# Kernel optimization log

Measured on AMD Instinct MI355X. Metric: run time of the kernel, lower is better.

## Reference

```python
import jax, jax.numpy as jnp
import numpy as np

B, N, D, H, DK, DV = 2, 2048, 1024, 16, 64, 64
NEG = -1000000000.0
EPS = 1e-6


def setup_inputs() -> dict:
    key = jax.random.key(0)
    ks = jax.random.split(key, 8)
    s = 0.02
    return {
        "q": jax.random.normal(ks[0], (B, N, D), jnp.float32),
        "k": jax.random.normal(ks[1], (B, N, D), jnp.float32),
        "v": jax.random.normal(ks[2], (B, N, D), jnp.float32),
        "attn_mask": jnp.ones((B, N, N), jnp.int32),
        "Wq": jax.random.normal(ks[3], (D, H * DK), jnp.float32) * s,
        "Wk": jax.random.normal(ks[4], (D, H * DK), jnp.float32) * s,
        "Wv": jax.random.normal(ks[5], (D, H * DV), jnp.float32) * s,
        "Wo": jax.random.normal(ks[6], (H * DV, D), jnp.float32) * s,
        "gamma": jnp.ones((D,), jnp.float32),
        "beta": jnp.zeros((D,), jnp.float32),
    }


def reference(q, k, v, attn_mask, Wq, Wk, Wv, Wo, gamma, beta):
    b, n, _ = q.shape
    residual = q
    # project and split heads: (b, h, n, dk)
    qh = (q @ Wq).reshape(b, n, H, DK).transpose(0, 2, 1, 3)
    kh = (k @ Wk).reshape(b, n, H, DK).transpose(0, 2, 1, 3)
    vh = (v @ Wv).reshape(b, n, H, DV).transpose(0, 2, 1, 3)
    temperature = DK ** 0.5
    scores = jnp.einsum('bhnd,bhmd->bhnm', qh / temperature, kh)
    # external mask (masked where mask == 0), broadcast over heads
    scores = jnp.where(attn_mask[:, None, :, :] == 0, NEG, scores)
    # built-in causal mask (strictly upper triangle)
    causal = jnp.triu(jnp.ones((n, n), dtype=bool), k=1)
    scores = jnp.where(causal, NEG, scores)
    attn = jax.nn.softmax(scores, axis=-1)
    out = jnp.einsum('bhnm,bhmd->bnhd', attn, vh).reshape(b, n, H * DV)
    out = out @ Wo + residual
    # LayerNorm(eps=1e-6)
    mean = out.mean(-1, keepdims=True)
    var = ((out - mean) ** 2).mean(-1, keepdims=True)
    out = (out - mean) / jnp.sqrt(var + EPS) * gamma + beta
    return out, attn
```

## Files before the change

### kernel.cpp

```cpp
#include <hip/hip_runtime.h>
#include <hip/hip_bf16.h>
#include <stdint.h>

#define B_ 2
#define N_ 2048
#define D_ 1024
#define H_ 16
#define MM 4096
#define NN 1024
#define KK 1024

typedef __bf16 bf16;
typedef __bf16 bf16x8 __attribute__((ext_vector_type(8)));
typedef float f32x4 __attribute__((ext_vector_type(4)));

struct __align__(8) bf4 { bf16 v[4]; };

#define LDS_STRIDE 144

__global__ void k_wtt(const float* __restrict__ W, bf16* __restrict__ Wt) {
    __shared__ float t[32][33];
    int bx = blockIdx.x * 32, by = blockIdx.y * 32;
    int tx = threadIdx.x, ty = threadIdx.y;
#pragma unroll
    for (int j = 0; j < 32; j += 8)
        t[ty + j][tx] = W[(size_t)(by + ty + j) * 1024 + bx + tx];
    __syncthreads();
#pragma unroll
    for (int j = 0; j < 32; j += 8)
        Wt[(size_t)(bx + ty + j) * 1024 + by + tx] = (bf16)t[tx][ty + j];
}

__global__ __launch_bounds__(256) void k_bits(const int* __restrict__ mask,
                                              uint32_t* __restrict__ bits) {
    size_t flat = (size_t)blockIdx.x * 256 + threadIdx.x;
    int col = (int)(flat & (N_ - 1));
    int row = (int)((flat >> 11) & (N_ - 1));
    bool ok = (mask[flat] != 0) && (col <= row);
    unsigned long long bal = __ballot(ok);
    if ((threadIdx.x & 63) == 0)
        *(unsigned long long*)(bits + (flat >> 5)) = bal;
}

template <int MODE, bool AF32>
__global__ __launch_bounds__(256) void k_gemm(const void* __restrict__ Av,
                                              const bf16* __restrict__ Bt,
                                              bf16* __restrict__ Cb,
                                              float* __restrict__ Cf,
                                              const float* __restrict__ resid,
                                              float scale) {
    __shared__ __align__(16) char AsB[64 * LDS_STRIDE];
    __shared__ __align__(16) char BsB[128 * LDS_STRIDE];
    const int tid = threadIdx.x, lane = tid & 63, w = tid >> 6;
    const int g = lane >> 4, li = lane & 15;
    const int bm0 = blockIdx.x * 64, bn0 = blockIdx.y * 128;
    const int srow = tid >> 3, sc = tid & 7;
    const bf16* Ab = (const bf16*)Av;
    const float* Af = (const float*)Av;

    f32x4 zz = {0.f, 0.f, 0.f, 0.f};
    f32x4 acc[4][2];
#pragma unroll
    for (int mf = 0; mf < 4; ++mf)
#pragma unroll
        for (int nf = 0; nf < 2; ++nf) acc[mf][nf] = zz;

    f32x4 pa0[2], pa1[2];
    bf16x8 pab[2];
    bf16x8 pb[4];

    auto issueA = [&](int k0) {
        if constexpr (AF32) {
#pragma unroll
            for (int i = 0; i < 2; ++i) {
                const float* s = Af + (size_t)(bm0 + srow + 32 * i) * KK + k0 + sc * 8;
                pa0[i] = *(const f32x4*)s;
                pa1[i] = *(const f32x4*)(s + 4);
            }
        } else {
#pragma unroll
            for (int i = 0; i < 2; ++i)
                pab[i] = *(const bf16x8*)(Ab + (size_t)(bm0 + srow + 32 * i) * KK + k0 + sc * 8);
        }
    };
    auto issueB = [&](int k0) {
#pragma unroll
        for (int i = 0; i < 4; ++i)
            pb[i] = *(const bf16x8*)(Bt + (size_t)(bn0 + srow + 32 * i) * KK + k0 + sc * 8);
    };
    auto writeS = [&]() {
#pragma unroll
        for (int i = 0; i < 2; ++i) {
            bf16x8 t;
            if constexpr (AF32) {
#pragma unroll
                for (int j = 0; j < 4; ++j) {
                    t[j] = (bf16)pa0[i][j];
                    t[4 + j] = (bf16)pa1[i][j];
                }
            } else {
                t = pab[i];
            }
            *(bf16x8*)(AsB + (srow + 32 * i) * LDS_STRIDE + sc * 16) = t;
        }
#pragma unroll
        for (int i = 0; i < 4; ++i)
            *(bf16x8*)(BsB + (srow + 32 * i) * LDS_STRIDE + sc * 16) = pb[i];
    };

    issueA(0);
    issueB(0);
    for (int k0 = 0; k0 < KK; k0 += 64) {
        __syncthreads();
        writeS();
        int kn = (k0 + 64 < KK) ? k0 + 64 : k0;
        issueA(kn);
        issueB(kn);
        __syncthreads();
#pragma unroll
        for (int kk = 0; kk < 2; ++kk) {
            const int kb = kk * 64 + (g << 4);
            bf16x8 bfr[2];
#pragma unroll
            for (int nf = 0; nf < 2; ++nf) {
                int rn = w * 32 + nf * 16 + li;
                bfr[nf] = *(const bf16x8*)(BsB + rn * LDS_STRIDE + kb);
            }
#pragma unroll
            for (int mf = 0; mf < 4; ++mf) {
                int rm = mf * 16 + li;
                bf16x8 afr = *(const bf16x8*)(AsB + rm * LDS_STRIDE + kb);
                acc[mf][0] = __builtin_amdgcn_mfma_f32_16x16x32_bf16(
                    afr, bfr[0], acc[mf][0], 0, 0, 0);
                acc[mf][1] = __builtin_amdgcn_mfma_f32_16x16x32_bf16(
                    afr, bfr[1], acc[mf][1], 0, 0, 0);
            }
        }
    }
#pragma unroll
    for (int mf = 0; mf < 4; ++mf)
#pragma unroll
        for (int nf = 0; nf < 2; ++nf) {
            int n = bn0 + w * 32 + nf * 16 + li;
            int m0 = bm0 + mf * 16 + (g << 2);
            if (MODE == 0) {
#pragma unroll
                for (int r = 0; r < 4; ++r)
                    Cb[(size_t)(m0 + r) * NN + n] = (bf16)(acc[mf][nf][r] * scale);
            } else if (MODE == 1) {
                int bq = m0 >> 11, tok = m0 & (N_ - 1);
                int hh = n >> 6, dv = n & 63;
                bf4 val;
#pragma unroll
                for (int r = 0; r < 4; ++r) val.v[r] = (bf16)(acc[mf][nf][r] * scale);
                *(bf4*)(Cb + ((size_t)((bq * H_ + hh) * 64 + dv)) * N_ + tok) = val;
            } else {
#pragma unroll
                for (int r = 0; r < 4; ++r) {
                    size_t ix = (size_t)(m0 + r) * NN + n;
                    Cf[ix] = acc[mf][nf][r] + resid[ix];
                }
            }
        }
}

__global__ __launch_bounds__(256) void k_attn(const bf16* __restrict__ Qh,
                                              const bf16* __restrict__ Kh,
                                              const bf16* __restrict__ Vt,
                                              const uint32_t* __restrict__ bits,
                                              float* __restrict__ attnp,
                                              bf16* __restrict__ Ob) {
    __shared__ __align__(16) char Qs[64 * LDS_STRIDE];
    __shared__ __align__(16) char Ks[64 * LDS_STRIDE];
    __shared__ __align__(16) char Vs[64 * LDS_STRIDE];
    __shared__ __align__(16) char Ps[64 * LDS_STRIDE];
    const int tid = threadIdx.x, lane = tid & 63, w = tid >> 6;
    const int g = lane >> 4, li = lane & 15;
    const int p = blockIdx.x, h = blockIdx.y, b = blockIdx.z;
    const int srow = tid >> 3, sc = tid & 7;
    const int myrow = w * 16 + li;

    const size_t kbase = ((size_t)b * N_) * D_ + h * 64;
    const size_t vbase = ((size_t)(b * H_ + h) * 64) * N_;
    f32x4 zz = {0.f, 0.f, 0.f, 0.f};

    for (int half = 0; half < 2; ++half) {
        const int qt = half ? (31 - p) : p;
        const int i0 = qt << 6;
        const size_t abase = (((size_t)b * H_ + h) * N_ + i0) * (size_t)N_;

        __syncthreads();
        {
            const char* qsrc = (const char*)Qh +
                (kbase + (size_t)(i0 + srow) * D_ + sc * 8) * 2;
            bf16x8 t0 = *(const bf16x8*)qsrc;
            bf16x8 t1 = *(const bf16x8*)(qsrc + (size_t)32 * D_ * 2);
            *(bf16x8*)(Qs + srow * LDS_STRIDE + sc * 16) = t0;
            *(bf16x8*)(Qs + (srow + 32) * LDS_STRIDE + sc * 16) = t1;
        }
        const uint32_t* mrow = bits + (((size_t)b * N_ + i0 + myrow) << 6);

        float m = -1e30f, l = 0.f;
        bf16x8 ka, kb2;
        {
            const char* ks = (const char*)Kh + (kbase + (size_t)srow * D_ + sc * 8) * 2;
            ka = *(const bf16x8*)ks;
            kb2 = *(const bf16x8*)(ks + (size_t)32 * D_ * 2);
        }
        for (int jt = 0; jt <= qt; ++jt) {
            __syncthreads();
            *(bf16x8*)(Ks + srow * LDS_STRIDE + sc * 16) = ka;
            *(bf16x8*)(Ks + (srow + 32) * LDS_STRIDE + sc * 16) = kb2;
            {
                int jn = (jt < qt) ? jt + 1 : qt;
                const char* ks = (const char*)Kh +
                    (kbase + (size_t)(jn * 64 + srow) * D_ + sc * 8) * 2;
                ka = *(const bf16x8*)ks;
                kb2 = *(const bf16x8*)(ks + (size_t)32 * D_ * 2);
            }
            uint2 mw = *(const uint2*)(mrow + (jt << 1));
            __syncthreads();

            f32x4 s[4];
#pragma unroll
            for (int mf = 0; mf < 4; ++mf) s[mf] = zz;
#pragma unroll
            for (int kk = 0; kk < 2; ++kk) {
                const int kb = kk * 64 + (g << 4);
                bf16x8 qf = *(const bf16x8*)(Qs + myrow * LDS_STRIDE + kb);
#pragma unroll
                for (int mf = 0; mf < 4; ++mf) {
                    bf16x8 kf = *(const bf16x8*)(Ks + (mf * 16 + li) * LDS_STRIDE + kb);
                    s[mf] = __builtin_amdgcn_mfma_f32_16x16x32_bf16(kf, qf, s[mf], 0, 0, 0);
                }
            }
            float tmax = m;
#pragma unroll
            for (int mf = 0; mf < 4; ++mf) {
                uint32_t wsel = (mf < 2) ? mw.x : mw.y;
#pragma unroll
                for (int r = 0; r < 4; ++r) {
                    int sh = (mf & 1) * 16 + g * 4 + r;
                    float xv = ((wsel >> sh) & 1) ? s[mf][r] : -1e9f;
                    s[mf][r] = xv;
                    tmax = fmaxf(tmax, xv);
                }
            }
            tmax = fmaxf(tmax, __shfl_xor(tmax, 16));
            tmax = fmaxf(tmax, __shfl_xor(tmax, 32));
            float ps = 0.f;
#pragma unroll
            for (int mf = 0; mf < 4; ++mf)
#pragma unroll
                for (int r = 0; r < 4; ++r) ps += __expf(s[mf][r] - tmax);
            ps += __shfl_xor(ps, 16);
            ps += __shfl_xor(ps, 32);
            l = l * __expf(m - tmax) + ps;
            m = tmax;
        }
        const float linv = 1.0f / l;

        f32x4 oacc[4];
#pragma unroll
        for (int nf = 0; nf < 4; ++nf) oacc[nf] = zz;

        bf16x8 va, vb2;
        {
            const char* ks = (const char*)Kh + (kbase + (size_t)srow * D_ + sc * 8) * 2;
            ka = *(const bf16x8*)ks;
            kb2 = *(const bf16x8*)(ks + (size_t)32 * D_ * 2);
            const char* vs = (const char*)Vt + (vbase + (size_t)srow * N_ + sc * 8) * 2;
            va = *(const bf16x8*)vs;
            vb2 = *(const bf16x8*)(vs + (size_t)32 * N_ * 2);
        }
        for (int jt = 0; jt <= qt; ++jt) {
            __syncthreads();
            *(bf16x8*)(Ks + srow * LDS_STRIDE + sc * 16) = ka;
            *(bf16x8*)(Ks + (srow + 32) * LDS_STRIDE + sc * 16) = kb2;
            *(bf16x8*)(Vs + srow * LDS_STRIDE + sc * 16) = va;
            *(bf16x8*)(Vs + (srow + 32) * LDS_STRIDE + sc * 16) = vb2;
            {
                int jn = (jt < qt) ? jt + 1 : qt;
                const char* ks = (const char*)Kh +
                    (kbase + (size_t)(jn * 64 + srow) * D_ + sc * 8) * 2;
                ka = *(const bf16x8*)ks;
                kb2 = *(const bf16x8*)(ks + (size_t)32 * D_ * 2);
                const char* vs = (const char*)Vt +
                    (vbase + (size_t)srow * N_ + jn * 64 + sc * 8) * 2;
                va = *(const bf16x8*)vs;
                vb2 = *(const bf16x8*)(vs + (size_t)32 * N_ * 2);
            }
            uint2 mw = *(const uint2*)(mrow + (jt << 1));
            __syncthreads();

            f32x4 s[4];
#pragma unroll
            for (int mf = 0; mf < 4; ++mf) s[mf] = zz;
#pragma unroll
            for (int kk = 0; kk < 2; ++kk) {
                const int kb = kk * 64 + (g << 4);
                bf16x8 qf = *(const bf16x8*)(Qs + myrow * LDS_STRIDE + kb);
#pragma unroll
                for (int mf = 0; mf < 4; ++mf) {
                    bf16x8 kf = *(const bf16x8*)(Ks + (mf * 16 + li) * LDS_STRIDE + kb);
                    s[mf] = __builtin_amdgcn_mfma_f32_16x16x32_bf16(kf, qf, s[mf], 0, 0, 0);
                }
            }
#pragma unroll
            for (int mf = 0; mf < 4; ++mf) {
                uint32_t wsel = (mf < 2) ? mw.x : mw.y;
#pragma unroll
                for (int r = 0; r < 4; ++r) {
                    int sh = (mf & 1) * 16 + g * 4 + r;
                    float xv = ((wsel >> sh) & 1) ? s[mf][r] : -1e9f;
                    s[mf][r] = __expf(xv - m) * linv;
                }
                *(f32x4*)(attnp + abase + (size_t)myrow * N_ + (jt << 6) + mf * 16 + g * 4) = s[mf];
                bf4 pk;
#pragma unroll
                for (int r = 0; r < 4; ++r) pk.v[r] = (bf16)s[mf][r];
                *(bf4*)(Ps + myrow * LDS_STRIDE + (mf * 16 + g * 4) * 2) = pk;
            }
#pragma unroll
            for (int kk = 0; kk < 2; ++kk) {
                const int kb = kk * 64 + (g << 4);
                bf16x8 pf = *(const bf16x8*)(Ps + myrow * LDS_STRIDE + kb);
#pragma unroll
                for (int nf = 0; nf < 4; ++nf) {
                    bf16x8 vf = *(const bf16x8*)(Vs + (nf * 16 + li) * LDS_STRIDE + kb);
                    oacc[nf] = __builtin_amdgcn_mfma_f32_16x16x32_bf16(pf, vf, oacc[nf], 0, 0, 0);
                }
            }
        }
#pragma unroll
        for (int nf = 0; nf < 4; ++nf)
#pragma unroll
            for (int r = 0; r < 4; ++r) {
                int gi = i0 + w * 16 + g * 4 + r;
                Ob[((size_t)(b * N_ + gi)) * D_ + h * 64 + nf * 16 + li] = (bf16)oacc[nf][r];
            }
        int zc0 = i0 + 64;
        if (zc0 < N_) {
            int r = tid >> 2, tc = tid & 3;
            f32x4 z = zz;
            for (int c = zc0 + tc * 4; c < N_; c += 16)
                *(f32x4*)(attnp + abase + (size_t)r * N_ + c) = z;
        }
    }
}

__global__ __launch_bounds__(256) void k_ln(float* __restrict__ out,
                                            const float* __restrict__ gamma,
                                            const float* __restrict__ beta) {
    const int row = blockIdx.x, t = threadIdx.x, lane = t & 63, w = t >> 6;
    float* p = out + (size_t)row * D_;
    f32x4 x = *(const f32x4*)(p + t * 4);
    float s = x[0] + x[1] + x[2] + x[3];
    float s2 = x[0] * x[0] + x[1] * x[1] + x[2] * x[2] + x[3] * x[3];
#pragma unroll
    for (int o = 1; o < 64; o <<= 1) {
        s += __shfl_xor(s, o);
        s2 += __shfl_xor(s2, o);
    }
    __shared__ float r1[4], r2[4];
    if (lane == 0) { r1[w] = s; r2[w] = s2; }
    __syncthreads();
    s = r1[0] + r1[1] + r1[2] + r1[3];
    s2 = r2[0] + r2[1] + r2[2] + r2[3];
    float mean = s * (1.f / D_);
    float var = s2 * (1.f / D_) - mean * mean;
    float rstd = rsqrtf(var + 1e-6f);
    f32x4 gv = *(const f32x4*)(gamma + t * 4);
    f32x4 bv = *(const f32x4*)(beta + t * 4);
    f32x4 y;
#pragma unroll
    for (int c = 0; c < 4; ++c) y[c] = (x[c] - mean) * rstd * gv[c] + bv[c];
    *(f32x4*)(p + t * 4) = y;
}

extern "C" void kernel_launch(void* const* d_in, const int* in_sizes, int n_in,
                              void* d_out, int out_size, void* d_ws,
                              size_t ws_size, hipStream_t stream) {
    (void)in_sizes; (void)n_in; (void)out_size; (void)ws_size;
    const float* q = (const float*)d_in[0];
    const float* k = (const float*)d_in[1];
    const float* v = (const float*)d_in[2];
    const int* msk = (const int*)d_in[3];
    const float* Wq = (const float*)d_in[4];
    const float* Wk = (const float*)d_in[5];
    const float* Wv = (const float*)d_in[6];
    const float* Wo = (const float*)d_in[7];
    const float* gamma = (const float*)d_in[8];
    const float* beta = (const float*)d_in[9];

    float* outp = (float*)d_out;
    float* attnp = outp + (size_t)B_ * N_ * D_;

    const size_t U = (size_t)B_ * N_ * D_;
    const size_t W1 = (size_t)D_ * D_;
    bf16* ws = (bf16*)d_ws;
    bf16* WqT = ws;  ws += W1;
    bf16* WkT = ws;  ws += W1;
    bf16* WvT = ws;  ws += W1;
    bf16* WoT = ws;  ws += W1;
    bf16* Qh = ws;   ws += U;
    bf16* Kh = ws;   ws += U;
    bf16* Vt = ws;   ws += U;
    bf16* Ob = ws;   ws += U;
    uint32_t* bits = (uint32_t*)ws;

    dim3 tb(32, 8);
    k_wtt<<<dim3(32, 32), tb, 0, stream>>>(Wq, WqT);
    k_wtt<<<dim3(32, 32), tb, 0, stream>>>(Wk, WkT);
    k_wtt<<<dim3(32, 32), tb, 0, stream>>>(Wv, WvT);
    k_wtt<<<dim3(32, 32), tb, 0, stream>>>(Wo, WoT);
    k_bits<<<(size_t)B_ * N_ * N_ / 256, 256, 0, stream>>>(msk, bits);

    dim3 gg(MM / 64, NN / 128);
    k_gemm<0, true><<<gg, 256, 0, stream>>>(q, WqT, Qh, nullptr, nullptr, 0.125f);
    k_gemm<0, true><<<gg, 256, 0, stream>>>(k, WkT, Kh, nullptr, nullptr, 1.0f);
    k_gemm<1, true><<<gg, 256, 0, stream>>>(v, WvT, Vt, nullptr, nullptr, 1.0f);

    k_attn<<<dim3(16, H_, B_), 256, 0, stream>>>(Qh, Kh, Vt, bits, attnp, Ob);

    k_gemm<2, false><<<gg, 256, 0, stream>>>(Ob, WoT, nullptr, outp, q, 1.0f);

    k_ln<<<B_ * N_, 256, 0, stream>>>(outp, gamma, beta);
}
```

Measured before the change: 285.9 us.

## Widen attention KV tile to 128, use exp2 softmax, fuse weight transposes

Each attention inner iteration now processes 128 key/value columns instead of 64. This halves the loop trips and the barrier pairs per tile, and gives more MFMA work per synchronisation. Softmax moves to exp2 by folding log2(e) into the Q scale, and normalisation is folded into the exponent through m+log2(l), which removes a multiply. The four weight-transpose launches become one 3D-grid launch. The cost is higher LDS and register use, which may lower occupancy, plus extra masked work on the last 128-wide tile. The zero-fill start also moves to the 128-aligned boundary.

Result: faster. 278.8 us, median of 3 (-2.5%).

```diff
diff --git a/kernel.cpp b/kernel.cpp
--- a/kernel.cpp
+++ b/kernel.cpp
@@ -17,8 +17,16 @@
 struct __align__(8) bf4 { bf16 v[4]; };
 
 #define LDS_STRIDE 144
-
-__global__ void k_wtt(const float* __restrict__ W, bf16* __restrict__ Wt) {
+#define PSTR 272
+#define LOG2E 1.44269504088896340736f
+
+__global__ void k_wtt4(const float* __restrict__ Wq, const float* __restrict__ Wk,
+                       const float* __restrict__ Wv, const float* __restrict__ Wo,
+                       bf16* __restrict__ WqT, bf16* __restrict__ WkT,
+                       bf16* __restrict__ WvT, bf16* __restrict__ WoT) {
+    const int z = blockIdx.z;
+    const float* W = z == 0 ? Wq : z == 1 ? Wk : z == 2 ? Wv : Wo;
+    bf16* Wt = z == 0 ? WqT : z == 1 ? WkT : z == 2 ? WvT : WoT;
     __shared__ float t[32][33];
     int bx = blockIdx.x * 32, by = blockIdx.y * 32;
     int tx = threadIdx.x, ty = threadIdx.y;
@@ -171,9 +179,9 @@
                                               float* __restrict__ attnp,
                                               bf16* __restrict__ Ob) {
     __shared__ __align__(16) char Qs[64 * LDS_STRIDE];
-    __shared__ __align__(16) char Ks[64 * LDS_STRIDE];
-    __shared__ __align__(16) char Vs[64 * LDS_STRIDE];
-    __shared__ __align__(16) char Ps[64 * LDS_STRIDE];
+    __shared__ __align__(16) char Ks[128 * LDS_STRIDE];
+    __shared__ __align__(16) char Vs[64 * PSTR];
+    __shared__ __align__(16) char Ps[64 * PSTR];
     const int tid = threadIdx.x, lane = tid & 63, w = tid >> 6;
     const int g = lane >> 4, li = lane & 15;
     const int p = blockIdx.x, h = blockIdx.y, b = blockIdx.z;
@@ -184,60 +192,77 @@
     const size_t vbase = ((size_t)(b * H_ + h) * 64) * N_;
     f32x4 zz = {0.f, 0.f, 0.f, 0.f};
 
+    bf16x8 kr[4], vr[4];
+    auto loadK = [&](int jt) {
+#pragma unroll
+        for (int i = 0; i < 4; ++i)
+            kr[i] = *(const bf16x8*)(Kh + kbase +
+                (size_t)(jt * 128 + srow + 32 * i) * D_ + sc * 8);
+    };
+    auto writeK = [&]() {
+#pragma unroll
+        for (int i = 0; i < 4; ++i)
+            *(bf16x8*)(Ks + (srow + 32 * i) * LDS_STRIDE + sc * 16) = kr[i];
+    };
+    auto loadV = [&](int jt) {
+#pragma unroll
+        for (int c = 0; c < 4; ++c) {
+            int row = srow + 32 * (c & 1);
+            int cc = sc + 8 * (c >> 1);
+            vr[c] = *(const bf16x8*)(Vt + vbase + (size_t)row * N_ + jt * 128 + cc * 8);
+        }
+    };
+    auto writeV = [&]() {
+#pragma unroll
+        for (int c = 0; c < 4; ++c) {
+            int row = srow + 32 * (c & 1);
+            int cc = sc + 8 * (c >> 1);
+            *(bf16x8*)(Vs + row * PSTR + cc * 16) = vr[c];
+        }
+    };
+
     for (int half = 0; half < 2; ++half) {
         const int qt = half ? (31 - p) : p;
         const int i0 = qt << 6;
+        const int R = (qt + 2) >> 1;
         const size_t abase = (((size_t)b * H_ + h) * N_ + i0) * (size_t)N_;
 
         __syncthreads();
         {
-            const char* qsrc = (const char*)Qh +
-                (kbase + (size_t)(i0 + srow) * D_ + sc * 8) * 2;
+            const bf16* qsrc = Qh + kbase + (size_t)(i0 + srow) * D_ + sc * 8;
             bf16x8 t0 = *(const bf16x8*)qsrc;
-            bf16x8 t1 = *(const bf16x8*)(qsrc + (size_t)32 * D_ * 2);
+            bf16x8 t1 = *(const bf16x8*)(qsrc + (size_t)32 * D_);
             *(bf16x8*)(Qs + srow * LDS_STRIDE + sc * 16) = t0;
             *(bf16x8*)(Qs + (srow + 32) * LDS_STRIDE + sc * 16) = t1;
         }
         const uint32_t* mrow = bits + (((size_t)b * N_ + i0 + myrow) << 6);
 
         float m = -1e30f, l = 0.f;
-        bf16x8 ka, kb2;
-        {
-            const char* ks = (const char*)Kh + (kbase + (size_t)srow * D_ + sc * 8) * 2;
-            ka = *(const bf16x8*)ks;
-            kb2 = *(const bf16x8*)(ks + (size_t)32 * D_ * 2);
-        }
-        for (int jt = 0; jt <= qt; ++jt) {
+        loadK(0);
+        for (int jt = 0; jt < R; ++jt) {
             __syncthreads();
-            *(bf16x8*)(Ks + srow * LDS_STRIDE + sc * 16) = ka;
-            *(bf16x8*)(Ks + (srow + 32) * LDS_STRIDE + sc * 16) = kb2;
-            {
-                int jn = (jt < qt) ? jt + 1 : qt;
-                const char* ks = (const char*)Kh +
-                    (kbase + (size_t)(jn * 64 + srow) * D_ + sc * 8) * 2;
-                ka = *(const bf16x8*)ks;
-                kb2 = *(const bf16x8*)(ks + (size_t)32 * D_ * 2);
-            }
-            uint2 mw = *(const uint2*)(mrow + (jt << 1));
+            writeK();
+            loadK((jt + 1 < R) ? jt + 1 : jt);
+            uint4 mw = *(const uint4*)(mrow + (jt << 2));
             __syncthreads();
 
-            f32x4 s[4];
-#pragma unroll
-            for (int mf = 0; mf < 4; ++mf) s[mf] = zz;
+            f32x4 s[8];
+#pragma unroll
+            for (int mf = 0; mf < 8; ++mf) s[mf] = zz;
 #pragma unroll
             for (int kk = 0; kk < 2; ++kk) {
                 const int kb = kk * 64 + (g << 4);
                 bf16x8 qf = *(const bf16x8*)(Qs + myrow * LDS_STRIDE + kb);
 #pragma unroll
-                for (int mf = 0; mf < 4; ++mf) {
+                for (int mf = 0; mf < 8; ++mf) {
                     bf16x8 kf = *(const bf16x8*)(Ks + (mf * 16 + li) * LDS_STRIDE + kb);
                     s[mf] = __builtin_amdgcn_mfma_f32_16x16x32_bf16(kf, qf, s[mf], 0, 0, 0);
                 }
             }
             float tmax = m;
 #pragma unroll
-            for (int mf = 0; mf < 4; ++mf) {
-                uint32_t wsel = (mf < 2) ? mw.x : mw.y;
+            for (int mf = 0; mf < 8; ++mf) {
+                uint32_t wsel = (mf < 2) ? mw.x : (mf < 4) ? mw.y : (mf < 6) ? mw.z : mw.w;
 #pragma unroll
                 for (int r = 0; r < 4; ++r) {
                     int sh = (mf & 1) * 16 + g * 4 + r;
@@ -250,84 +275,70 @@
             tmax = fmaxf(tmax, __shfl_xor(tmax, 32));
             float ps = 0.f;
 #pragma unroll
-            for (int mf = 0; mf < 4; ++mf)
-#pragma unroll
-                for (int r = 0; r < 4; ++r) ps += __expf(s[mf][r] - tmax);
+            for (int mf = 0; mf < 8; ++mf)
+#pragma unroll
+                for (int r = 0; r < 4; ++r) ps += exp2f(s[mf][r] - tmax);
             ps += __shfl_xor(ps, 16);
             ps += __shfl_xor(ps, 32);
-            l = l * __expf(m - tmax) + ps;
+            l = l * exp2f(m - tmax) + ps;
             m = tmax;
         }
-        const float linv = 1.0f / l;
+        const float ml = m + __log2f(l);
 
         f32x4 oacc[4];
 #pragma unroll
         for (int nf = 0; nf < 4; ++nf) oacc[nf] = zz;
 
-        bf16x8 va, vb2;
-        {
-            const char* ks = (const char*)Kh + (kbase + (size_t)srow * D_ + sc * 8) * 2;
-            ka = *(const bf16x8*)ks;
-            kb2 = *(const bf16x8*)(ks + (size_t)32 * D_ * 2);
-            const char* vs = (const char*)Vt + (vbase + (size_t)srow * N_ + sc * 8) * 2;
-            va = *(const bf16x8*)vs;
-            vb2 = *(const bf16x8*)(vs + (size_t)32 * N_ * 2);
-        }
-        for (int jt = 0; jt <= qt; ++jt) {
+        loadK(0);
+        loadV(0);
+        for (int jt = 0; jt < R; ++jt) {
             __syncthreads();
-            *(bf16x8*)(Ks + srow * LDS_STRIDE + sc * 16) = ka;
-            *(bf16x8*)(Ks + (srow + 32) * LDS_STRIDE + sc * 16) = kb2;
-            *(bf16x8*)(Vs + srow * LDS_STRIDE + sc * 16) = va;
-            *(bf16x8*)(Vs + (srow + 32) * LDS_STRIDE + sc * 16) = vb2;
+            writeK();
+            writeV();
             {
-                int jn = (jt < qt) ? jt + 1 : qt;
-                const char* ks = (const char*)Kh +
-                    (kbase + (size_t)(jn * 64 + srow) * D_ + sc * 8) * 2;
-                ka = *(const bf16x8*)ks;
-                kb2 = *(const bf16x8*)(ks + (size_t)32 * D_ * 2);
-                const char* vs = (const char*)Vt +
-                    (vbase + (size_t)srow * N_ + jn * 64 + sc * 8) * 2;
-                va = *(const bf16x8*)vs;
-                vb2 = *(const bf16x8*)(vs + (size_t)32 * N_ * 2);
-            }
-            uint2 mw = *(const uint2*)(mrow + (jt << 1));
+                int jn = (jt + 1 < R) ? jt + 1 : jt;
+                loadK(jn);
+                loadV(jn);
+            }
+            uint4 mw = *(const uint4*)(mrow + (jt << 2));
             __syncthreads();
 
-            f32x4 s[4];
-#pragma unroll
-            for (int mf = 0; mf < 4; ++mf) s[mf] = zz;
+            f32x4 s[8];
+#pragma unroll
+            for (int mf = 0; mf < 8; ++mf) s[mf] = zz;
 #pragma unroll
             for (int kk = 0; kk < 2; ++kk) {
                 const int kb = kk * 64 + (g << 4);
                 bf16x8 qf = *(const bf16x8*)(Qs + myrow * LDS_STRIDE + kb);
 #pragma unroll
-                for (int mf = 0; mf < 4; ++mf) {
+                for (int mf = 0; mf < 8; ++mf) {
                     bf16x8 kf = *(const bf16x8*)(Ks + (mf * 16 + li) * LDS_STRIDE + kb);
                     s[mf] = __builtin_amdgcn_mfma_f32_16x16x32_bf16(kf, qf, s[mf], 0, 0, 0);
                 }
             }
-#pragma unroll
-            for (int mf = 0; mf < 4; ++mf) {
-                uint32_t wsel = (mf < 2) ? mw.x : mw.y;
+
+#pragma unroll
+            for (int mf = 0; mf < 8; ++mf) {
+                uint32_t wsel = (mf < 2) ? mw.x : (mf < 4) ? mw.y : (mf < 6) ? mw.z : mw.w;
 #pragma unroll
                 for (int r = 0; r < 4; ++r) {
                     int sh = (mf & 1) * 16 + g * 4 + r;
                     float xv = ((wsel >> sh) & 1) ? s[mf][r] : -1e9f;
-                    s[mf][r] = __expf(xv - m) * linv;
-                }
-                *(f32x4*)(attnp + abase + (size_t)myrow * N_ + (jt << 6) + mf * 16 + g * 4) = s[mf];
+                    s[mf][r] = exp2f(xv - ml);
+                }
+                *(f32x4*)(attnp + abase + (size_t)myrow * N_ + (jt << 7) + mf * 16 + g * 4) = s[mf];
                 bf4 pk;
 #pragma unroll
                 for (int r = 0; r < 4; ++r) pk.v[r] = (bf16)s[mf][r];
-                *(bf4*)(Ps + myrow * LDS_STRIDE + (mf * 16 + g * 4) * 2) = pk;
-            }
-#pragma unroll
-            for (int kk = 0; kk < 2; ++kk) {
+                *(bf4*)(Ps + myrow * PSTR + (mf * 16 + g * 4) * 2) = pk;
+            }
+#pragma unroll
+            for (int kk = 0; kk < 4; ++kk) {
                 const int kb = kk * 64 + (g << 4);
-                bf16x8 pf = *(const bf16x8*)(Ps + myrow * LDS_STRIDE + kb);
+                bf16x8 pf = *(const bf16x8*)(Ps + myrow * PSTR + kb);
 #pragma unroll
                 for (int nf = 0; nf < 4; ++nf) {
-                    bf16x8 vf = *(const bf16x8*)(Vs + (nf * 16 + li) * LDS_STRIDE + kb);
+                    bf16x8 vf = *(const bf16x8*)(Vs + (nf * 16 + li) * PSTR + kb);
                     oacc[nf] = __builtin_amdgcn_mfma_f32_16x16x32_bf16(pf, vf, oacc[nf], 0, 0, 0);
                 }
             }
@@ -339,7 +350,7 @@
                 int gi = i0 + w * 16 + g * 4 + r;
                 Ob[((size_t)(b * N_ + gi)) * D_ + h * 64 + nf * 16 + li] = (bf16)oacc[nf][r];
             }
-        int zc0 = i0 + 64;
+        int zc0 = R << 7;
         if (zc0 < N_) {
             int r = tid >> 2, tc = tid & 3;
             f32x4 z = zz;
@@ -409,15 +420,11 @@
     bf16* Ob = ws;   ws += U;
     uint32_t* bits = (uint32_t*)ws;
 
-    dim3 tb(32, 8);
-    k_wtt<<<dim3(32, 32), tb, 0, stream>>>(Wq, WqT);
-    k_wtt<<<dim3(32, 32), tb, 0, stream>>>(Wk, WkT);
-    k_wtt<<<dim3(32, 32), tb, 0, stream>>>(Wv, WvT);
-    k_wtt<<<dim3(32, 32), tb, 0, stream>>>(Wo, WoT);
+    k_wtt4<<<dim3(32, 32, 4), dim3(32, 8), 0, stream>>>(Wq, Wk, Wv, Wo, WqT, WkT, WvT, WoT);
     k_bits<<<(size_t)B_ * N_ * N_ / 256, 256, 0, stream>>>(msk, bits);
 
     dim3 gg(MM / 64, NN / 128);
-    k_gemm<0, true><<<gg, 256, 0, stream>>>(q, WqT, Qh, nullptr, nullptr, 0.125f);
+    k_gemm<0, true><<<gg, 256, 0, stream>>>(q, WqT, Qh, nullptr, nullptr, 0.125f * LOG2E);
     k_gemm<0, true><<<gg, 256, 0, stream>>>(k, WkT, Kh, nullptr, nullptr, 1.0f);
     k_gemm<1, true><<<gg, 256, 0, stream>>>(v, WvT, Vt, nullptr, nullptr, 1.0f);
 
```
